# Kernel optimization log

Measured on AMD Instinct MI355X. Metric: run time of the kernel, lower is better.

## Reference

```python
import jax, jax.numpy as jnp
import numpy as np

INPUT_DIM = 1024
HIDDEN_DIM = 1024
OUTPUT_DIM = 1024
NUM_HEADS = 16
HEAD_DIM = HIDDEN_DIM // NUM_HEADS


def setup_inputs() -> dict:
    key = jax.random.key(0)
    ks = jax.random.split(key, 9)
    s = 1.0 / np.sqrt(INPUT_DIM)
    so = 1.0 / np.sqrt(HIDDEN_DIM)
    x = jax.random.normal(ks[0], (4, 2048, INPUT_DIM), dtype=jnp.float32)
    Wq = jax.random.uniform(ks[1], (INPUT_DIM, HIDDEN_DIM), minval=-s, maxval=s, dtype=jnp.float32)
    bq = jax.random.uniform(ks[2], (HIDDEN_DIM,), minval=-s, maxval=s, dtype=jnp.float32)
    Wk = jax.random.uniform(ks[3], (INPUT_DIM, HIDDEN_DIM), minval=-s, maxval=s, dtype=jnp.float32)
    bk = jax.random.uniform(ks[4], (HIDDEN_DIM,), minval=-s, maxval=s, dtype=jnp.float32)
    Wv = jax.random.uniform(ks[5], (INPUT_DIM, HIDDEN_DIM), minval=-s, maxval=s, dtype=jnp.float32)
    bv = jax.random.uniform(ks[6], (HIDDEN_DIM,), minval=-s, maxval=s, dtype=jnp.float32)
    Wo = jax.random.uniform(ks[7], (HIDDEN_DIM, OUTPUT_DIM), minval=-so, maxval=so, dtype=jnp.float32)
    bo = jax.random.uniform(ks[8], (OUTPUT_DIM,), minval=-so, maxval=so, dtype=jnp.float32)
    return {"x": x, "Wq": Wq, "bq": bq, "Wk": Wk, "bk": bk, "Wv": Wv, "bv": bv, "Wo": Wo, "bo": bo}


def reference(x, Wq, bq, Wk, bk, Wv, bv, Wo, bo):
    B, S, _ = x.shape
    H, D = NUM_HEADS, HEAD_DIM
    # project and split heads -> [B, H, S, D]
    Q = (x @ Wq + bq).reshape(B, S, H, D).transpose(0, 2, 1, 3)
    K = (x @ Wk + bk).reshape(B, S, H, D).transpose(0, 2, 1, 3)
    V = (x @ Wv + bv).reshape(B, S, H, D).transpose(0, 2, 1, 3)
    scores = jnp.einsum('bhsd,bhtd->bhst', Q, K) / jnp.sqrt(jnp.asarray(D, x.dtype))
    attn = jax.nn.softmax(scores, axis=-1)
    out = jnp.einsum('bhst,bhtd->bhsd', attn, V)  # [B, H, S, D]
    out = out.transpose(0, 2, 1, 3).reshape(B, S, H * D)
    return out @ Wo + bo
```

## Files before the change

### kernel.cpp

```cpp
#include <hip/hip_runtime.h>

#define DI __device__ __forceinline__

typedef __bf16 bf16x8 __attribute__((ext_vector_type(8)));
typedef float f32x4 __attribute__((ext_vector_type(4)));
typedef float f32x16 __attribute__((ext_vector_type(16)));
typedef unsigned u32;
typedef u32 u32x2v __attribute__((ext_vector_type(2)));
typedef u32 u32x4v __attribute__((ext_vector_type(4)));

#define QSCALE 0.180336880111f

DI ushort f2bf(float f) {
  unsigned u = __builtin_bit_cast(unsigned, f);
  unsigned r = (u + 0x7FFFu + ((u >> 16) & 1u)) >> 16;
  return (ushort)r;
}

DI void gload_lds16(const void* g, void* l) {
  __builtin_amdgcn_global_load_lds(
      (const __attribute__((address_space(1))) unsigned*)g,
      (__attribute__((address_space(3))) unsigned*)l, 16, 0, 0);
}

DI bf16x8 load_frag(const ushort* p) { return *(const bf16x8*)p; }

DI u32 cvtpk(float lo, float hi) {
  u32 r;
  asm("v_cvt_pk_bf16_f32 %0, %1, %2" : "=v"(r) : "v"(lo), "v"(hi));
  return r;
}

#if defined(__has_builtin)
#if __has_builtin(__builtin_amdgcn_permlane32_swap)
#define HAVE_PLSWAP 1
#endif
#endif

DI u32x2v permswap(u32 a, u32 b) {
#ifdef HAVE_PLSWAP
  return __builtin_amdgcn_permlane32_swap(a, b, false, false);
#else
  int hi = (threadIdx.x >> 5) & 1;
  u32 bl = __shfl_xor(b, 32, 64);
  u32 ah = __shfl_xor(a, 32, 64);
  u32x2v r;
  r[0] = hi ? bl : a;
  r[1] = hi ? b : ah;
  return r;
#endif
}

DI f32x16 mfma32(bf16x8 a, bf16x8 b, f32x16 c) {
  return __builtin_amdgcn_mfma_f32_32x32x16_bf16(a, b, c, 0, 0, 0);
}

__global__ __launch_bounds__(256) void k_convert_x(const float* __restrict__ x,
                                                   ushort* __restrict__ xb) {
  int i = (blockIdx.x * 256 + threadIdx.x) * 4;
  float4 v = *(const float4*)(x + i);
  ushort4 o;
  o.x = f2bf(v.x); o.y = f2bf(v.y); o.z = f2bf(v.z); o.w = f2bf(v.w);
  *(ushort4*)(xb + i) = o;
}

__global__ __launch_bounds__(256) void k_transpose_w4(
    const float* __restrict__ W0, const float* __restrict__ W1,
    const float* __restrict__ W2, const float* __restrict__ W3,
    ushort* __restrict__ T0, ushort* __restrict__ T1,
    ushort* __restrict__ T2, ushort* __restrict__ T3) {
  __shared__ float tile[64][65];
  int which = blockIdx.x >> 8;
  int bt = blockIdx.x & 255;
  const float* W = which == 0 ? W0 : which == 1 ? W1 : which == 2 ? W2 : W3;
  ushort* Wt = which == 0 ? T0 : which == 1 ? T1 : which == 2 ? T2 : T3;
  int k0 = (bt & 15) << 6;
  int n0 = (bt >> 4) << 6;
  int c = threadIdx.x & 63;
  int r0 = threadIdx.x >> 6;
#pragma unroll
  for (int i = 0; i < 16; ++i) {
    int r = i * 4 + r0;
    tile[r][c] = W[(k0 + r) * 1024 + n0 + c];
  }
  __syncthreads();
#pragma unroll
  for (int i = 0; i < 16; ++i) {
    int nn = i * 4 + r0;
    Wt[(n0 + nn) * 1024 + k0 + c] = f2bf(tile[c][nn]);
  }
}

__global__ __launch_bounds__(256, 2) void k_gemm_qkv(
    const ushort* __restrict__ A, const ushort* __restrict__ Bt3,
    const float* __restrict__ bq, const float* __restrict__ bk,
    const float* __restrict__ bv, ushort* __restrict__ Qb,
    ushort* __restrict__ Kb, ushort* __restrict__ Vtb) {
  __shared__ ushort Asm[8192];
  __shared__ ushort Bsm[8192];
  int L = blockIdx.x;
  int xcd = L & 7;
  int i0 = L >> 3;
  int chunk = i0 >> 6;
  int j = i0 & 63;
  int brow = xcd * 8 + (j & 7);
  int bcol = chunk * 8 + (j >> 3);
  int which = bcol >> 3;
  int colb = bcol & 7;
  int tid = threadIdx.x;
  int w = tid >> 6, lane = tid & 63;
  int g = lane >> 4, lr = lane & 15;
  int wr = w >> 1, wc = w & 1;
  const char* Abase = (const char*)(A + (size_t)brow * 128 * 1024);
  const char* Bbase = (const char*)(Bt3 + (size_t)bcol * 128 * 1024);
  f32x4 acc[4][4] = {};
  for (int kt = 0; kt < 16; ++kt) {
    int k0b = kt * 128;
#pragma unroll
    for (int i = 0; i < 4; ++i) {
      int jj = w * 4 + i;
      int fo = jj * 1024 + lane * 16;
      int row = fo >> 7;
      int cis = ((fo >> 4) & 7) ^ (row & 7);
      long srcoff = (long)row * 2048 + k0b + cis * 16;
      gload_lds16(Abase + srcoff, (char*)Asm + jj * 1024);
      gload_lds16(Bbase + srcoff, (char*)Bsm + jj * 1024);
    }
    __syncthreads();
#pragma unroll
    for (int ks = 0; ks < 2; ++ks) {
      bf16x8 af[4], bfr[4];
#pragma unroll
      for (int m = 0; m < 4; ++m) {
        int row = wr * 64 + m * 16 + lr;
        int ci = (ks * 4 + g) ^ (row & 7);
        af[m] = *(const bf16x8*)((const char*)Asm + row * 128 + ci * 16);
      }
#pragma unroll
      for (int n = 0; n < 4; ++n) {
        int row = wc * 64 + n * 16 + lr;
        int ci = (ks * 4 + g) ^ (row & 7);
        bfr[n] = *(const bf16x8*)((const char*)Bsm + row * 128 + ci * 16);
      }
#pragma unroll
      for (int m = 0; m < 4; ++m)
#pragma unroll
        for (int n = 0; n < 4; ++n)
          acc[m][n] = __builtin_amdgcn_mfma_f32_16x16x32_bf16(af[m], bfr[n], acc[m][n], 0, 0, 0);
    }
    __syncthreads();
  }
  const float* bp = which == 0 ? bq : which == 1 ? bk : bv;
  float osc = which == 0 ? QSCALE : 1.0f;
#pragma unroll
  for (int m = 0; m < 4; ++m) {
#pragma unroll
    for (int n = 0; n < 4; ++n) {
      int c = colb * 128 + wc * 64 + n * 16 + lr;
      float bvv = bp[c];
      int h = c >> 6, d = c & 63;
#pragma unroll
      for (int r = 0; r < 4; ++r) {
        int R = brow * 128 + wr * 64 + m * 16 + g * 4 + r;
        int b = R >> 11, s = R & 2047;
        float v = (acc[m][n][r] + bvv) * osc;
        if (which == 0)
          Qb[(((size_t)(b * 16 + h) * 2048 + s) << 6) + d] = f2bf(v);
        else if (which == 1)
          Kb[(((size_t)(b * 16 + h) * 2048 + s) << 6) + d] = f2bf(v);
        else
          Vtb[(((size_t)(b * 16 + h) * 64 + d) << 11) + s] = f2bf(v);
      }
    }
  }
}

__global__ __launch_bounds__(256, 2) void k_gemm_o(const ushort* __restrict__ A,
                                                   const ushort* __restrict__ Bt,
                                                   const float* __restrict__ bias,
                                                   float* __restrict__ out) {
  __shared__ ushort Asm[8192];
  __shared__ ushort Bsm[8192];
  int L = blockIdx.x;
  int xcd = L & 7;
  int j = L >> 3;
  int brow = xcd * 8 + (j & 7);
  int bcol = j >> 3;
  int tid = threadIdx.x;
  int w = tid >> 6, lane = tid & 63;
  int g = lane >> 4, lr = lane & 15;
  int wr = w >> 1, wc = w & 1;
  const char* Abase = (const char*)(A + (size_t)brow * 128 * 1024);
  const char* Bbase = (const char*)(Bt + (size_t)bcol * 128 * 1024);
  f32x4 acc[4][4] = {};
  for (int kt = 0; kt < 16; ++kt) {
    int k0b = kt * 128;
#pragma unroll
    for (int i = 0; i < 4; ++i) {
      int jj = w * 4 + i;
      int fo = jj * 1024 + lane * 16;
      int row = fo >> 7;
      int cis = ((fo >> 4) & 7) ^ (row & 7);
      long srcoff = (long)row * 2048 + k0b + cis * 16;
      gload_lds16(Abase + srcoff, (char*)Asm + jj * 1024);
      gload_lds16(Bbase + srcoff, (char*)Bsm + jj * 1024);
    }
    __syncthreads();
#pragma unroll
    for (int ks = 0; ks < 2; ++ks) {
      bf16x8 af[4], bfr[4];
#pragma unroll
      for (int m = 0; m < 4; ++m) {
        int row = wr * 64 + m * 16 + lr;
        int ci = (ks * 4 + g) ^ (row & 7);
        af[m] = *(const bf16x8*)((const char*)Asm + row * 128 + ci * 16);
      }
#pragma unroll
      for (int n = 0; n < 4; ++n) {
        int row = wc * 64 + n * 16 + lr;
        int ci = (ks * 4 + g) ^ (row & 7);
        bfr[n] = *(const bf16x8*)((const char*)Bsm + row * 128 + ci * 16);
      }
#pragma unroll
      for (int m = 0; m < 4; ++m)
#pragma unroll
        for (int n = 0; n < 4; ++n)
          acc[m][n] = __builtin_amdgcn_mfma_f32_16x16x32_bf16(af[m], bfr[n], acc[m][n], 0, 0, 0);
    }
    __syncthreads();
  }
#pragma unroll
  for (int m = 0; m < 4; ++m) {
#pragma unroll
    for (int n = 0; n < 4; ++n) {
      int Cc = bcol * 128 + wc * 64 + n * 16 + lr;
      float bvv = bias[Cc];
#pragma unroll
      for (int r = 0; r < 4; ++r) {
        int R = brow * 128 + wr * 64 + m * 16 + g * 4 + r;
        out[(size_t)R * 1024 + Cc] = acc[m][n][r] + bvv;
      }
    }
  }
}

DI void stage2(const char* Kp, const char* Vp, char* Kd, char* Vd, int t0,
               int w, int lane) {
#pragma unroll
  for (int i = 0; i < 2; ++i) {
    int j = w * 2 + i;
    int fo = j * 1024 + lane * 16;
    int row = fo >> 7;
    int ch = ((fo >> 4) & 7) ^ (row & 7);
    gload_lds16(Kp + (size_t)(t0 + row) * 128 + ch * 16, Kd + j * 1024);
    gload_lds16(Vp + (size_t)row * 4096 + (size_t)t0 * 2 + ch * 16, Vd + j * 1024);
  }
}

#define PACKP(pp, base, dst)                                \
  {                                                         \
    u32 a0 = cvtpk(pp[(base) + 0], pp[(base) + 1]);         \
    u32 b0 = cvtpk(pp[(base) + 4], pp[(base) + 5]);         \
    u32 a1 = cvtpk(pp[(base) + 2], pp[(base) + 3]);         \
    u32 b1 = cvtpk(pp[(base) + 6], pp[(base) + 7]);         \
    u32x2v r0 = permswap(a0, b0);                           \
    u32x2v r1 = permswap(a1, b1);                           \
    u32x4v f;                                               \
    f.x = r0.x; f.y = r1.x; f.z = r0.y; f.w = r1.y;         \
    dst = __builtin_bit_cast(bf16x8, f);                    \
  }

__global__ __launch_bounds__(256, 2) void k_attn(const ushort* __restrict__ Qb,
                                                 const ushort* __restrict__ Kb,
                                                 const ushort* __restrict__ Vt,
                                                 ushort* __restrict__ aout) {
  __shared__ ushort Ksm[3][4096];
  __shared__ ushort Vsm[3][4096];
  int L = blockIdx.x;
  int xcd = L & 7, idx = L >> 3;
  int bh = xcd * 8 + (idx >> 3);
  int qt = idx & 7;
  int b = bh >> 4, h = bh & 15;
  int tid = threadIdx.x;
  int w = tid >> 6, lane = tid & 63, l31 = lane & 31, hi = lane >> 5;
  const ushort* Qp = Qb + (size_t)bh * 2048 * 64;
  const char* Kp = (const char*)(Kb + (size_t)bh * 2048 * 64);
  const char* Vp = (const char*)(Vt + (size_t)bh * 64 * 2048);

  int q0 = qt * 256 + w * 64;
  bf16x8 qf0[4], qf1[4];
#pragma unroll
  for (int ks = 0; ks < 4; ++ks) {
    qf0[ks] = load_frag(Qp + (q0 + l31) * 64 + ks * 16 + hi * 8);
    qf1[ks] = load_frag(Qp + (q0 + 32 + l31) * 64 + ks * 16 + hi * 8);
  }
  f32x16 o00 = {}, o01 = {}, o10 = {}, o11 = {};
  f32x16 sAcc0 = {}, sAcc1 = {};
  u32x4v onesu;
  onesu.x = 0x3F803F80u; onesu.y = 0x3F803F80u;
  onesu.z = 0x3F803F80u; onesu.w = 0x3F803F80u;
  bf16x8 onesf = __builtin_bit_cast(bf16x8, onesu);

  char *kA = (char*)Ksm[0], *kB = (char*)Ksm[1], *kC = (char*)Ksm[2];
  char *vA = (char*)Vsm[0], *vB = (char*)Vsm[1], *vC = (char*)Vsm[2];
  stage2(Kp, Vp, kA, vA, 0, w, lane);
  stage2(Kp, Vp, kB, vB, 64, w, lane);

  for (int t = 0; t < 32; ++t) {
    asm volatile("s_waitcnt vmcnt(4)" ::: "memory");
    __builtin_amdgcn_s_barrier();
    int nt = t + 2;
    if (nt >= 32) nt -= 32;
    stage2(Kp, Vp, kC, vC, nt * 64, w, lane);
    const char* Kc = kA;
    const char* Vc = vA;
    f32x16 s00 = {}, s01 = {};
    __builtin_amdgcn_s_setprio(1);
#pragma unroll
    for (int ks = 0; ks < 4; ++ks) {
      int ci = ((ks * 2 + hi) ^ (l31 & 7)) << 4;
      bf16x8 ka = *(const bf16x8*)(Kc + l31 * 128 + ci);
      s00 = mfma32(ka, qf0[ks], s00);
      s01 = mfma32(ka, qf1[ks], s01);
    }
    __builtin_amdgcn_s_setprio(0);
#pragma unroll
    for (int i = 0; i < 16; ++i) {
      s00[i] = __builtin_amdgcn_exp2f(s00[i]);
      s01[i] = __builtin_amdgcn_exp2f(s01[i]);
    }
    bf16x8 pA0, pA1, pA2, pA3, pB0, pB1, pB2, pB3;
    PACKP(s00, 0, pA0); PACKP(s00, 8, pA1);
    PACKP(s01, 0, pB0); PACKP(s01, 8, pB1);
    f32x16 s10 = {}, s11 = {};
    __builtin_amdgcn_s_setprio(1);
#pragma unroll
    for (int ks = 0; ks < 4; ++ks) {
      int ci = ((ks * 2 + hi) ^ (l31 & 7)) << 4;
      bf16x8 ka = *(const bf16x8*)(Kc + (32 + l31) * 128 + ci);
      s10 = mfma32(ka, qf0[ks], s10);
      s11 = mfma32(ka, qf1[ks], s11);
    }
    __builtin_amdgcn_s_setprio(0);
#pragma unroll
    for (int i = 0; i < 16; ++i) {
      s10[i] = __builtin_amdgcn_exp2f(s10[i]);
      s11[i] = __builtin_amdgcn_exp2f(s11[i]);
    }
    PACKP(s10, 0, pA2); PACKP(s10, 8, pA3);
    PACKP(s11, 0, pB2); PACKP(s11, 8, pB3);
    __builtin_amdgcn_s_setprio(1);
#pragma unroll
    for (int ks = 0; ks < 4; ++ks) {
      int ci = ((ks * 2 + hi) ^ (l31 & 7)) << 4;
      bf16x8 va0 = *(const bf16x8*)(Vc + l31 * 128 + ci);
      bf16x8 va1 = *(const bf16x8*)(Vc + (32 + l31) * 128 + ci);
      bf16x8 pa = (ks == 0) ? pA0 : (ks == 1) ? pA1 : (ks == 2) ? pA2 : pA3;
      bf16x8 pb = (ks == 0) ? pB0 : (ks == 1) ? pB1 : (ks == 2) ? pB2 : pB3;
      o00 = mfma32(va0, pa, o00);
      o10 = mfma32(va1, pa, o10);
      o01 = mfma32(va0, pb, o01);
      o11 = mfma32(va1, pb, o11);
      sAcc0 = mfma32(onesf, pa, sAcc0);
      sAcc1 = mfma32(onesf, pb, sAcc1);
    }
    __builtin_amdgcn_s_setprio(0);
    char* tk = kA; kA = kB; kB = kC; kC = tk;
    char* tv = vA; vA = vB; vB = vC; vC = tv;
  }
  float rl0 = 1.f / sAcc0[0];
  float rl1 = 1.f / sAcc1[0];
  ushort* orow0 = aout + ((size_t)b * 2048 + q0 + l31) * 1024 + h * 64;
  ushort* orow1 = aout + ((size_t)b * 2048 + q0 + 32 + l31) * 1024 + h * 64;
#pragma unroll
  for (int r = 0; r < 8; ++r) {
    int d0 = ((2 * r) & 3) + 8 * ((2 * r) >> 2) + 4 * hi;
    *(u32*)(orow0 + d0)      = cvtpk(o00[2 * r] * rl0, o00[2 * r + 1] * rl0);
    *(u32*)(orow0 + 32 + d0) = cvtpk(o10[2 * r] * rl0, o10[2 * r + 1] * rl0);
    *(u32*)(orow1 + d0)      = cvtpk(o01[2 * r] * rl1, o01[2 * r + 1] * rl1);
    *(u32*)(orow1 + 32 + d0) = cvtpk(o11[2 * r] * rl1, o11[2 * r + 1] * rl1);
  }
}

extern "C" void kernel_launch(void* const* d_in, const int* in_sizes, int n_in,
                              void* d_out, int out_size, void* d_ws, size_t ws_size,
                              hipStream_t stream) {
  const float* x  = (const float*)d_in[0];
  const float* Wq = (const float*)d_in[1];
  const float* bq = (const float*)d_in[2];
  const float* Wk = (const float*)d_in[3];
  const float* bk = (const float*)d_in[4];
  const float* Wv = (const float*)d_in[5];
  const float* bv = (const float*)d_in[6];
  const float* Wo = (const float*)d_in[7];
  const float* bo = (const float*)d_in[8];
  char* wsb = (char*)d_ws;
  ushort* xb   = (ushort*)(wsb);
  ushort* WqT  = (ushort*)(wsb + (16u << 20));
  ushort* WkT  = (ushort*)(wsb + (18u << 20));
  ushort* WvT  = (ushort*)(wsb + (20u << 20));
  ushort* WoT  = (ushort*)(wsb + (22u << 20));
  ushort* Qb   = (ushort*)(wsb + (24u << 20));
  ushort* Kb   = (ushort*)(wsb + (40u << 20));
  ushort* Vtb  = (ushort*)(wsb + (56u << 20));
  ushort* aout = xb;

  k_convert_x<<<8192, 256, 0, stream>>>(x, xb);
  k_transpose_w4<<<1024, 256, 0, stream>>>(Wq, Wk, Wv, Wo, WqT, WkT, WvT, WoT);
  k_gemm_qkv<<<1536, 256, 0, stream>>>(xb, WqT, bq, bk, bv, Qb, Kb, Vtb);
  k_attn<<<512, 256, 0, stream>>>(Qb, Kb, Vtb, aout);
  k_gemm_o<<<512, 256, 0, stream>>>(aout, WoT, bo, (float*)d_out);
}
```

Measured before the change: 260.5 us.

## Rework QKV GEMM into 256x256 tiles with double-buffered async LDS pipeline

The QKV projection GEMM moves from 128x128 tiles with 256 threads to 256x256 tiles with 512 threads (8 waves, each computing 128x64). It cuts K-steps to 64 and double-buffers the LDS tiles, issuing the next global-to-LDS loads while the MFMAs run. It also raises wave priority around the MFMA block. The goal is to hide global-load latency and raise operand reuse per byte loaded, at the cost of more registers and LDS per block and only 384 blocks, which may leave some CUs idle.

```diff
diff --git a/kernel.cpp b/kernel.cpp
--- a/kernel.cpp
+++ b/kernel.cpp
@@ -91,77 +91,91 @@
   }
 }
 
-__global__ __launch_bounds__(256, 2) void k_gemm_qkv(
+__global__ __launch_bounds__(512, 2) void k_gemm_qkv(
     const ushort* __restrict__ A, const ushort* __restrict__ Bt3,
     const float* __restrict__ bq, const float* __restrict__ bk,
     const float* __restrict__ bv, ushort* __restrict__ Qb,
     ushort* __restrict__ Kb, ushort* __restrict__ Vtb) {
-  __shared__ ushort Asm[8192];
-  __shared__ ushort Bsm[8192];
+  __shared__ ushort As[2][8192];
+  __shared__ ushort Bs[2][8192];
   int L = blockIdx.x;
   int xcd = L & 7;
   int i0 = L >> 3;
-  int chunk = i0 >> 6;
-  int j = i0 & 63;
-  int brow = xcd * 8 + (j & 7);
-  int bcol = chunk * 8 + (j >> 3);
-  int which = bcol >> 3;
-  int colb = bcol & 7;
+  int brow = xcd * 4 + (i0 & 3);
+  int bcol = i0 >> 2;
   int tid = threadIdx.x;
   int w = tid >> 6, lane = tid & 63;
   int g = lane >> 4, lr = lane & 15;
-  int wr = w >> 1, wc = w & 1;
-  const char* Abase = (const char*)(A + (size_t)brow * 128 * 1024);
-  const char* Bbase = (const char*)(Bt3 + (size_t)bcol * 128 * 1024);
-  f32x4 acc[4][4] = {};
-  for (int kt = 0; kt < 16; ++kt) {
-    int k0b = kt * 128;
-#pragma unroll
-    for (int i = 0; i < 4; ++i) {
-      int jj = w * 4 + i;
-      int fo = jj * 1024 + lane * 16;
-      int row = fo >> 7;
-      int cis = ((fo >> 4) & 7) ^ (row & 7);
-      long srcoff = (long)row * 2048 + k0b + cis * 16;
-      gload_lds16(Abase + srcoff, (char*)Asm + jj * 1024);
-      gload_lds16(Bbase + srcoff, (char*)Bsm + jj * 1024);
-    }
-    __syncthreads();
-#pragma unroll
-    for (int ks = 0; ks < 2; ++ks) {
-      bf16x8 af[4], bfr[4];
-#pragma unroll
-      for (int m = 0; m < 4; ++m) {
-        int row = wr * 64 + m * 16 + lr;
-        int ci = (ks * 4 + g) ^ (row & 7);
-        af[m] = *(const bf16x8*)((const char*)Asm + row * 128 + ci * 16);
-      }
-#pragma unroll
-      for (int n = 0; n < 4; ++n) {
-        int row = wc * 64 + n * 16 + lr;
-        int ci = (ks * 4 + g) ^ (row & 7);
-        bfr[n] = *(const bf16x8*)((const char*)Bsm + row * 128 + ci * 16);
-      }
-#pragma unroll
-      for (int m = 0; m < 4; ++m)
-#pragma unroll
-        for (int n = 0; n < 4; ++n)
-          acc[m][n] = __builtin_amdgcn_mfma_f32_16x16x32_bf16(af[m], bfr[n], acc[m][n], 0, 0, 0);
-    }
-    __syncthreads();
-  }
+  int wr = w >> 2, wc = w & 3;
+  const char* Abase = (const char*)(A + (size_t)brow * 256 * 1024);
+  const char* Bbase = (const char*)(Bt3 + (size_t)bcol * 256 * 1024);
+
+  int slot = w * 2;
+  int fo0 = slot * 1024 + lane * 16;
+  int fo1 = fo0 + 1024;
+  int row0 = fo0 >> 6, ch0 = (fo0 >> 4) & 3;
+  int row1 = fo1 >> 6, ch1 = (fo1 >> 4) & 3;
+  long aoff0 = (long)row0 * 2048 + ((ch0 ^ (row0 & 3)) << 4);
+  long aoff1 = (long)row1 * 2048 + ((ch1 ^ (row1 & 3)) << 4);
+
+#define STAGE_QKV(buf, kt)                                            \
+  {                                                                   \
+    long kb = (long)(kt) * 64;                                        \
+    gload_lds16(Abase + aoff0 + kb, (char*)As[buf] + slot * 1024);    \
+    gload_lds16(Abase + aoff1 + kb, (char*)As[buf] + slot * 1024 + 1024); \
+    gload_lds16(Bbase + aoff0 + kb, (char*)Bs[buf] + slot * 1024);    \
+    gload_lds16(Bbase + aoff1 + kb, (char*)Bs[buf] + slot * 1024 + 1024); \
+  }
+
+  f32x4 acc[8][4] = {};
+  STAGE_QKV(0, 0);
+  STAGE_QKV(1, 1);
+
+  for (int kt = 0; kt < 32; ++kt) {
+    int pb = kt & 1;
+    asm volatile("s_waitcnt vmcnt(4)" ::: "memory");
+    __builtin_amdgcn_s_barrier();
+    const char* Ac = (const char*)As[pb];
+    const char* Bc = (const char*)Bs[pb];
+    bf16x8 af[8], bf[4];
+#pragma unroll
+    for (int m = 0; m < 8; ++m) {
+      int row = wr * 128 + m * 16 + lr;
+      af[m] = *(const bf16x8*)(Ac + row * 64 + ((g ^ (row & 3)) << 4));
+    }
+#pragma unroll
+    for (int n = 0; n < 4; ++n) {
+      int row = wc * 64 + n * 16 + lr;
+      bf[n] = *(const bf16x8*)(Bc + row * 64 + ((g ^ (row & 3)) << 4));
+    }
+    asm volatile("s_waitcnt lgkmcnt(0)" ::: "memory");
+    __builtin_amdgcn_sched_barrier(0);
+    __builtin_amdgcn_s_barrier();
+    int nt = kt + 2;
+    if (nt >= 32) nt -= 32;
+    STAGE_QKV(pb, nt);
+    __builtin_amdgcn_s_setprio(1);
+#pragma unroll
+    for (int m = 0; m < 8; ++m)
+#pragma unroll
+      for (int n = 0; n < 4; ++n)
+        acc[m][n] = __builtin_amdgcn_mfma_f32_16x16x32_bf16(af[m], bf[n], acc[m][n], 0, 0, 0);
+    __builtin_amdgcn_s_setprio(0);
+  }
+
+  int which = bcol >> 2;
   const float* bp = which == 0 ? bq : which == 1 ? bk : bv;
   float osc = which == 0 ? QSCALE : 1.0f;
 #pragma unroll
-  for (int m = 0; m < 4; ++m) {
+  for (int m = 0; m < 8; ++m) {
 #pragma unroll
     for (int n = 0; n < 4; ++n) {
-      int c = colb * 128 + wc * 64 + n * 16 + lr;
+      int c = (bcol & 3) * 256 + wc * 64 + n * 16 + lr;
       float bvv = bp[c];
       int h = c >> 6, d = c & 63;
 #pragma unroll
       for (int r = 0; r < 4; ++r) {
-        int R = brow * 128 + wr * 64 + m * 16 + g * 4 + r;
+        int R = brow * 256 + wr * 128 + m * 16 + g * 4 + r;
         int b = R >> 11, s = R & 2047;
         float v = (acc[m][n][r] + bvv) * osc;
         if (which == 0)
@@ -407,7 +421,7 @@
 
   k_convert_x<<<8192, 256, 0, stream>>>(x, xb);
   k_transpose_w4<<<1024, 256, 0, stream>>>(Wq, Wk, Wv, Wo, WqT, WkT, WvT, WoT);
-  k_gemm_qkv<<<1536, 256, 0, stream>>>(xb, WqT, bq, bk, bv, Qb, Kb, Vtb);
+  k_gemm_qkv<<<384, 512, 0, stream>>>(xb, WqT, bq, bk, bv, Qb, Kb, Vtb);
   k_attn<<<512, 256, 0, stream>>>(Qb, Kb, Vtb, aout);
   k_gemm_o<<<512, 256, 0, stream>>>(aout, WoT, bo, (float*)d_out);
 }
```

After: 302.0 us. 1.16x slower.
